# Performance work log

Measured on AMD Instinct MI355X. Metric: run time of the kernel, lower is better.

The kernel has to match this reference:

```python
import jax, jax.numpy as jnp
import numpy as np


def setup_inputs() -> dict:
    key = jax.random.key(0)
    k1, k2 = jax.random.split(key)
    set1 = jax.random.normal(k1, (8, 4096, 3), dtype=jnp.float32)
    set2 = jax.random.normal(k2, (8, 4096, 3), dtype=jnp.float32)
    return {"set1": set1, "set2": set2}


def reference(set1, set2):
    # set1: [b, n, d], set2: [b, m, d]
    n = set1.shape[1]
    x2 = jnp.sum(set1 * set1, axis=-1)            # [b, n]
    y2 = jnp.sum(set2 * set2, axis=-1)            # [b, m]
    xy = jnp.einsum('bnd,bmd->bnm', set1, set2)   # [b, n, m]
    d2 = x2[:, :, None] + y2[:, None, :] - 2.0 * xy
    dist = jnp.sqrt(jnp.maximum(d2, 0.0))         # torch.cdist(p=2)
    out_dist = jnp.min(dist, axis=2)              # [b, n]
    out_dist2 = jnp.min(dist, axis=1)             # [b, m]
    total = jnp.mean(out_dist) + jnp.mean(out_dist2)
    return total / n
```

## Files before the change

### kernel.cpp

```cpp
#include <hip/hip_runtime.h>
#include <math.h>
#include <float.h>


#define BATCH   8
#define NPTS    4096
#define THREADS 512
#define QB      128
#define QPT     4
#define NGRP    16
#define PPG     (NPTS/NGRP)

__global__ __launch_bounds__(THREADS, 4)
void chamfer_main(const float* __restrict__ set1,
                  const float* __restrict__ set2,
                  float* __restrict__ out)
{
    __shared__ float4 dbp[NPTS];
    __shared__ float  part[NGRP][QB];

    const int blk = blockIdx.x;
    const int dir = blk >> 8;
    const int rem = blk & 255;
    const int b   = rem >> 5;
    const int qb  = rem & 31;

    const float* __restrict__ Q  = dir ? set2 : set1;
    const float* __restrict__ DB = dir ? set1 : set2;
    const float* __restrict__ DBb = DB + (size_t)b * NPTS * 3;

    const int t = threadIdx.x;

    for (int i = t; i < NPTS; i += THREADS) {
        const float x = DBb[3 * i + 0];
        const float y = DBb[3 * i + 1];
        const float z = DBb[3 * i + 2];
        dbp[i] = make_float4(x, y, z, fmaf(x, x, fmaf(y, y, z * z)));
    }

    const int l = t & 31;
    const int g = t >> 5;
    const int qbase = qb * QB;

    float qa[QPT], qbc[QPT], qc[QPT], dmin[QPT];
    #pragma unroll
    for (int j = 0; j < QPT; ++j) {
        const float* qp = Q + ((size_t)b * NPTS + qbase + l + 32 * j) * 3;
        qa[j]  = -2.0f * qp[0];
        qbc[j] = -2.0f * qp[1];
        qc[j]  = -2.0f * qp[2];
        dmin[j] = FLT_MAX;
    }

    __syncthreads();

    const float4* __restrict__ s4 = dbp + g * PPG;

    #pragma unroll 2
    for (int c = 0; c < PPG / 4; ++c) {
        const float4 P0 = s4[c * 4 + 0];
        const float4 P1 = s4[c * 4 + 1];
        const float4 P2 = s4[c * 4 + 2];
        const float4 P3 = s4[c * 4 + 3];
        #pragma unroll
        for (int j = 0; j < QPT; ++j) {
            const float a = qa[j], bb = qbc[j], cc = qc[j];
            float d0 = fmaf(a, P0.x, fmaf(bb, P0.y, fmaf(cc, P0.z, P0.w)));
            float d1 = fmaf(a, P1.x, fmaf(bb, P1.y, fmaf(cc, P1.z, P1.w)));
            float d2 = fmaf(a, P2.x, fmaf(bb, P2.y, fmaf(cc, P2.z, P2.w)));
            float d3 = fmaf(a, P3.x, fmaf(bb, P3.y, fmaf(cc, P3.z, P3.w)));
            dmin[j] = fminf(dmin[j], fminf(fminf(d0, d1), fminf(d2, d3)));
        }
    }

    #pragma unroll
    for (int j = 0; j < QPT; ++j)
        part[g][l + 32 * j] = dmin[j];
    __syncthreads();

    float dist = 0.0f;
    if (t < QB) {
        float m = part[0][t];
        #pragma unroll
        for (int gg = 1; gg < NGRP; ++gg)
            m = fminf(m, part[gg][t]);
        const float* qp = Q + ((size_t)b * NPTS + qbase + t) * 3;
        const float qx = qp[0], qy = qp[1], qz = qp[2];
        const float q2 = fmaf(qx, qx, fmaf(qy, qy, qz * qz));
        dist = sqrtf(fmaxf(q2 + m, 0.0f));
    }

    #pragma unroll
    for (int off = 32; off > 0; off >>= 1)
        dist += __shfl_down(dist, off);
    if (t < QB && (t & 63) == 0)
        atomicAdd(out, dist * (1.0f / (float)((size_t)BATCH * NPTS * NPTS)));
}

extern "C" void kernel_launch(void* const* d_in, const int* in_sizes, int n_in,
                              void* d_out, int out_size, void* d_ws, size_t ws_size,
                              hipStream_t stream) {
    const float* s1 = (const float*)d_in[0];
    const float* s2 = (const float*)d_in[1];
    float* out = (float*)d_out;

    hipMemsetAsync(out, 0, sizeof(float), stream);
    chamfer_main<<<dim3(512), dim3(THREADS), 0, stream>>>(s1, s2, out);
}
```

Baseline: 82.95 us.

## Prepack points into float4 workspace and read database via wave-uniform global loads

Adds a pre-pass kernel that packs both point sets into float4 (x,y,z,|p|^2) in workspace, so the main kernel no longer stages the database in LDS. Each wave takes a contiguous slice of database points through wave-uniform (scalar-friendly) global loads, reorganising the work to 64-lane waves with 2 queries per thread. The goal is to remove the per-block LDS fill, the __syncthreads before compute, and LDS read traffic, and to cut the partial-min reduction from 16 groups to 8. The costs are an extra kernel launch, workspace round-trip traffic, and fewer queries per thread, which means less reuse of each loaded point.

Measured after the change: 99.94 us. 1.2x slower.

```diff
diff --git a/kernel.cpp b/kernel.cpp
--- a/kernel.cpp
+++ b/kernel.cpp
@@ -7,87 +7,90 @@
 #define NPTS    4096
 #define THREADS 512
 #define QB      128
-#define QPT     4
-#define NGRP    16
-#define PPG     (NPTS/NGRP)
+#define QPT     2
+#define NWAVES  8
+#define PPW     (NPTS/NWAVES)
+
+__global__ __launch_bounds__(256)
+void pack_pts(const float* __restrict__ set1,
+              const float* __restrict__ set2,
+              float4* __restrict__ pk)
+{
+    const int i = blockIdx.x * 256 + threadIdx.x;
+    const float* __restrict__ src = (i < BATCH * NPTS) ? set1 : set2;
+    const int idx = i & (BATCH * NPTS - 1);
+    const float x = src[3 * idx + 0];
+    const float y = src[3 * idx + 1];
+    const float z = src[3 * idx + 2];
+    pk[i] = make_float4(x, y, z, fmaf(x, x, fmaf(y, y, z * z)));
+}
 
 __global__ __launch_bounds__(THREADS, 4)
-void chamfer_main(const float* __restrict__ set1,
-                  const float* __restrict__ set2,
+void chamfer_main(const float4* __restrict__ pk,
                   float* __restrict__ out)
 {
-    __shared__ float4 dbp[NPTS];
-    __shared__ float  part[NGRP][QB];
+    __shared__ float part[NWAVES][QB];
 
     const int blk = blockIdx.x;
     const int dir = blk >> 8;
     const int rem = blk & 255;
     const int b   = rem >> 5;
-    const int qb  = rem & 31;
+    const int qc  = rem & 31;
+    const int qbase = qc * QB;
 
-    const float* __restrict__ Q  = dir ? set2 : set1;
-    const float* __restrict__ DB = dir ? set1 : set2;
-    const float* __restrict__ DBb = DB + (size_t)b * NPTS * 3;
+    const float4* __restrict__ Qb  = pk + (dir ? BATCH * NPTS : 0) + (size_t)b * NPTS;
+    const float4* __restrict__ DBb = pk + (dir ? 0 : BATCH * NPTS) + (size_t)b * NPTS;
 
-    const int t = threadIdx.x;
+    const int t    = threadIdx.x;
+    const int lane = t & 63;
+    const int w    = __builtin_amdgcn_readfirstlane(t >> 6);
 
-    for (int i = t; i < NPTS; i += THREADS) {
-        const float x = DBb[3 * i + 0];
-        const float y = DBb[3 * i + 1];
-        const float z = DBb[3 * i + 2];
-        dbp[i] = make_float4(x, y, z, fmaf(x, x, fmaf(y, y, z * z)));
-    }
-
-    const int l = t & 31;
-    const int g = t >> 5;
-    const int qbase = qb * QB;
-
-    float qa[QPT], qbc[QPT], qc[QPT], dmin[QPT];
+    float qa[QPT], qbv[QPT], qcv[QPT], dmin[QPT];
     #pragma unroll
     for (int j = 0; j < QPT; ++j) {
-        const float* qp = Q + ((size_t)b * NPTS + qbase + l + 32 * j) * 3;
-        qa[j]  = -2.0f * qp[0];
-        qbc[j] = -2.0f * qp[1];
-        qc[j]  = -2.0f * qp[2];
+        const float4 q = Qb[qbase + lane + 64 * j];
+        qa[j]  = -2.0f * q.x;
+        qbv[j] = -2.0f * q.y;
+        qcv[j] = -2.0f * q.z;
         dmin[j] = FLT_MAX;
     }
 
-    __syncthreads();
+    const float4* __restrict__ P = DBb + w * PPW;
 
-    const float4* __restrict__ s4 = dbp + g * PPG;
-
-    #pragma unroll 2
-    for (int c = 0; c < PPG / 4; ++c) {
-        const float4 P0 = s4[c * 4 + 0];
-        const float4 P1 = s4[c * 4 + 1];
-        const float4 P2 = s4[c * 4 + 2];
-        const float4 P3 = s4[c * 4 + 3];
+    for (int c = 0; c < PPW; c += 8) {
+        float d[QPT][8];
+        #pragma unroll
+        for (int k = 0; k < 8; ++k) {
+            const float4 p = P[c + k];
+            #pragma unroll
+            for (int j = 0; j < QPT; ++j) {
+                d[j][k] = fmaf(qa[j], p.x,
+                          fmaf(qbv[j], p.y,
+                          fmaf(qcv[j], p.z, p.w)));
+            }
+        }
         #pragma unroll
         for (int j = 0; j < QPT; ++j) {
-            const float a = qa[j], bb = qbc[j], cc = qc[j];
-            float d0 = fmaf(a, P0.x, fmaf(bb, P0.y, fmaf(cc, P0.z, P0.w)));
-            float d1 = fmaf(a, P1.x, fmaf(bb, P1.y, fmaf(cc, P1.z, P1.w)));
-            float d2 = fmaf(a, P2.x, fmaf(bb, P2.y, fmaf(cc, P2.z, P2.w)));
-            float d3 = fmaf(a, P3.x, fmaf(bb, P3.y, fmaf(cc, P3.z, P3.w)));
-            dmin[j] = fminf(dmin[j], fminf(fminf(d0, d1), fminf(d2, d3)));
+            const float m0 = fminf(fminf(d[j][0], d[j][1]), d[j][2]);
+            const float m1 = fminf(fminf(d[j][3], d[j][4]), m0);
+            const float m2 = fminf(fminf(d[j][5], d[j][6]), m1);
+            dmin[j] = fminf(fminf(d[j][7], m2), dmin[j]);
         }
     }
 
     #pragma unroll
     for (int j = 0; j < QPT; ++j)
-        part[g][l + 32 * j] = dmin[j];
+        part[w][lane + 64 * j] = dmin[j];
     __syncthreads();
 
     float dist = 0.0f;
     if (t < QB) {
         float m = part[0][t];
         #pragma unroll
-        for (int gg = 1; gg < NGRP; ++gg)
-            m = fminf(m, part[gg][t]);
-        const float* qp = Q + ((size_t)b * NPTS + qbase + t) * 3;
-        const float qx = qp[0], qy = qp[1], qz = qp[2];
-        const float q2 = fmaf(qx, qx, fmaf(qy, qy, qz * qz));
-        dist = sqrtf(fmaxf(q2 + m, 0.0f));
+        for (int ww = 1; ww < NWAVES; ++ww)
+            m = fminf(m, part[ww][t]);
+        const float4 q = Qb[qbase + t];
+        dist = sqrtf(fmaxf(q.w + m, 0.0f));
     }
 
     #pragma unroll
@@ -103,7 +106,9 @@
     const float* s1 = (const float*)d_in[0];
     const float* s2 = (const float*)d_in[1];
     float* out = (float*)d_out;
+    float4* pk = (float4*)d_ws;
 
     hipMemsetAsync(out, 0, sizeof(float), stream);
-    chamfer_main<<<dim3(512), dim3(THREADS), 0, stream>>>(s1, s2, out);
+    pack_pts<<<dim3((2 * BATCH * NPTS) / 256), dim3(256), 0, stream>>>(s1, s2, pk);
+    chamfer_main<<<dim3(512), dim3(THREADS), 0, stream>>>(pk, out);
 }
```
